# Optimization experiments

Measured on AMD Instinct MI355X. Metric: run time of the kernel, lower is better.

Reference implementation:

```python
import jax, jax.numpy as jnp
import numpy as np

K = 3
K2 = K * K


def conv2d(x, w, b, stride=1, pad=0):
    y = jax.lax.conv_general_dilated(
        x, w, (stride, stride), [(pad, pad), (pad, pad)],
        dimension_numbers=('NCHW', 'OIHW', 'NCHW'))
    return y + b[None, :, None, None]


def bilinear_gather(x, ys, xs):
    # x: [B,C,H,W]; ys,xs: [B,K2,H,W] float coords; zero outside bounds (torchvision deform_conv2d semantics)
    B, C, H, W = x.shape
    y0 = jnp.floor(ys)
    x0 = jnp.floor(xs)
    fy = (ys - y0)[:, None]  # [B,1,K2,H,W]
    fx = (xs - x0)[:, None]
    xf = x.reshape(B, C, H * W)

    def gather(yc, xc):
        valid = (yc >= 0) & (yc <= H - 1) & (xc >= 0) & (xc <= W - 1)
        yi = jnp.clip(yc, 0, H - 1).astype(jnp.int32)
        xi = jnp.clip(xc, 0, W - 1).astype(jnp.int32)
        idx = (yi * W + xi).reshape(B, 1, -1)
        g = jnp.take_along_axis(xf, idx, axis=2).reshape(B, C, K2, H, W)
        return g * valid[:, None].astype(x.dtype)

    g00 = gather(y0, x0)
    g01 = gather(y0, x0 + 1)
    g10 = gather(y0 + 1, x0)
    g11 = gather(y0 + 1, x0 + 1)
    return (g00 * (1 - fy) * (1 - fx) + g01 * (1 - fy) * fx
            + g10 * fy * (1 - fx) + g11 * fy * fx)


def deform_conv(x, w_off, b_off, w, b):
    # DCNv1: offsets predicted by a regular 3x3 conv, then 3x3 conv over bilinearly sampled taps
    B, C, H, W = x.shape
    pad = 1
    off = conv2d(x, w_off, b_off, pad=pad).reshape(B, K2, 2, H, W)  # (dy,dx) per tap
    ky, kx = jnp.meshgrid(jnp.arange(K), jnp.arange(K), indexing='ij')
    base_y = jnp.arange(H)[None, None, :, None] + (ky.reshape(K2) - pad)[None, :, None, None]
    base_x = jnp.arange(W)[None, None, None, :] + (kx.reshape(K2) - pad)[None, :, None, None]
    ys = base_y + off[:, :, 0]
    xs = base_x + off[:, :, 1]
    samples = bilinear_gather(x, ys, xs)  # [B,C,K2,H,W]
    out = jnp.einsum('bckhw,ock->bohw', samples, w.reshape(w.shape[0], C, K2))
    return out + b[None, :, None, None]


def band_high_mask(h, w):
    y, x = jnp.meshgrid(jnp.arange(h), jnp.arange(w), indexing='ij')
    d = jnp.sqrt(((y - h // 2) ** 2 + (x - w // 2) ** 2).astype(jnp.float32))
    return (d > h // 16).astype(jnp.float32)


def reference(x, w1, b1, ws, bs, wb, bb, woff, boff, wreg, breg, w2, b2):
    B, Cin, Hx, Wx = x.shape
    c0 = conv2d(x, w1, b1)                                  # 1x1 reduce
    c1 = conv2d(c0, ws, bs, stride=2, pad=0)                # 3x3 s2 p0 -> 111x111
    c1 = jax.lax.reduce_window(c1, -jnp.inf, jax.lax.max,
                               (1, 1, 7, 7), (1, 1, 3, 3), 'VALID')  # -> 35x35
    f = jnp.fft.fftshift(jnp.fft.fft2(c1, axes=(-2, -1)), axes=(-2, -1))
    mag = jnp.abs(f)
    phase = jnp.angle(f)
    h, w = mag.shape[-2], mag.shape[-1]
    hb = mag * band_high_mask(h, w)
    for l in range(3):  # fixed structural loop over the 3 DCN+ReLU blocks
        hb = jax.nn.relu(deform_conv(hb, woff[l], boff[l], wreg[l], breg[l]))
    rec = jax.lax.complex(hb * jnp.cos(phase), hb * jnp.sin(phase))
    rec = jnp.real(jnp.fft.ifft2(jnp.fft.ifftshift(rec, axes=(-2, -1)), axes=(-2, -1)))
    up = jax.image.resize(rec, (B, rec.shape[1], Hx, Wx), method='bilinear')  # align_corners=False
    c2 = jax.nn.sigmoid(conv2d(conv2d(c0, wb, bb) + up, w2, b2))
    return x * c2


def setup_inputs():
    key = jax.random.key(0)
    ks = jax.random.split(key, 8)
    B, Cin, H, W = 4, 256, 224, 224
    Cr = Cin // 8
    f32 = jnp.float32
    x = jax.random.normal(ks[0], (B, Cin, H, W), f32)
    w1 = jax.random.normal(ks[1], (Cr, Cin, 1, 1), f32) * 0.05
    b1 = jnp.zeros((Cr,), f32)
    ws = jax.random.normal(ks[2], (Cr, Cr, 3, 3), f32) * 0.05
    bs = jnp.zeros((Cr,), f32)
    wb = jax.random.normal(ks[3], (Cr, Cr, 1, 1), f32) * 0.05
    bb = jnp.zeros((Cr,), f32)
    woff = jax.random.normal(ks[4], (3, 2 * K2, Cr, 3, 3), f32) * 0.002  # small -> moderate offsets
    boff = jnp.zeros((3, 2 * K2), f32)
    wreg = jax.random.normal(ks[5], (3, Cr, Cr, 3, 3), f32) * 0.05
    breg = jnp.zeros((3, Cr), f32)
    w2 = jax.random.normal(ks[6], (Cin, Cr, 1, 1), f32) * 0.05
    b2 = jnp.zeros((Cin,), f32)
    return dict(x=x, w1=w1, b1=b1, ws=ws, bs=bs, wb=wb, bb=bb,
                woff=woff, boff=boff, wreg=wreg, breg=breg, w2=w2, b2=b2)
```

## Files before the change

### kernel.cpp

```cpp
#include <hip/hip_runtime.h>
#include <math.h>

#define PI_F 3.14159265358979323846f

#define BATCH 4
#define CIN 256
#define CR 32
#define H0 224
#define HW0 (224*224)
#define H1 111
#define HW1 (111*111)
#define HS 35
#define HWS (35*35)

typedef short bf16x8 __attribute__((ext_vector_type(8)));
typedef float f32x4 __attribute__((ext_vector_type(4)));
typedef unsigned int u32x4 __attribute__((ext_vector_type(4)));

__device__ inline unsigned pack2bf(float a, float b) {
  unsigned ua = __builtin_bit_cast(unsigned, a);
  unsigned ub = __builtin_bit_cast(unsigned, b);
  return ((ua + 0x8000u) >> 16) | (((ub + 0x8000u) & 0xFFFF0000u) | (((ub + 0x8000u) >> 16) << 16));
}

__device__ inline unsigned pack2(float a, float b) {
  unsigned ua = __builtin_bit_cast(unsigned, a);
  unsigned ub = __builtin_bit_cast(unsigned, b);
  return ((ua + 0x8000u) >> 16) | (((ub + 0x8000u) >> 16) << 16);
}

__device__ inline bf16x8 pack8(const float f[8]) {
  u32x4 u;
  u[0] = pack2(f[0], f[1]);
  u[1] = pack2(f[2], f[3]);
  u[2] = pack2(f[4], f[5]);
  u[3] = pack2(f[6], f[7]);
  return __builtin_bit_cast(bf16x8, u);
}

__global__ __launch_bounds__(256) void k_conv1x1(
    const float* __restrict__ x, const float* __restrict__ w1,
    const float* __restrict__ b1, float* __restrict__ c0) {
  int tid = threadIdx.x, lane = tid & 63, wid = tid >> 6;
  int l15 = lane & 15, lg = lane >> 4;
  int pxg = blockIdx.x * 256 + wid * 64;
  int b = pxg / HW0, p0 = pxg % HW0;
  bf16x8 A[2][8];
#pragma unroll
  for (int ct = 0; ct < 2; ++ct)
#pragma unroll
    for (int ks = 0; ks < 8; ++ks) {
      const float* wr = w1 + (ct * 16 + l15) * CIN + ks * 32 + lg * 8;
      float f[8];
      float4 a0 = *reinterpret_cast<const float4*>(wr);
      float4 a1 = *reinterpret_cast<const float4*>(wr + 4);
      f[0]=a0.x; f[1]=a0.y; f[2]=a0.z; f[3]=a0.w;
      f[4]=a1.x; f[5]=a1.y; f[6]=a1.z; f[7]=a1.w;
      A[ct][ks] = pack8(f);
    }
  f32x4 acc[2][4];
#pragma unroll
  for (int ct = 0; ct < 2; ++ct)
#pragma unroll
    for (int pt = 0; pt < 4; ++pt)
#pragma unroll
      for (int r = 0; r < 4; ++r) acc[ct][pt][r] = 0.f;
  const float* xb = x + (size_t)b * CIN * HW0 + p0 + l15;
  for (int ks = 0; ks < 8; ++ks) {
    bf16x8 Bf[4];
#pragma unroll
    for (int pt = 0; pt < 4; ++pt) {
      const float* xp = xb + (size_t)(ks * 32 + lg * 8) * HW0 + pt * 16;
      float f[8];
#pragma unroll
      for (int j = 0; j < 8; ++j) f[j] = xp[(size_t)j * HW0];
      Bf[pt] = pack8(f);
    }
#pragma unroll
    for (int ct = 0; ct < 2; ++ct)
#pragma unroll
      for (int pt = 0; pt < 4; ++pt)
        acc[ct][pt] = __builtin_amdgcn_mfma_f32_16x16x32_bf16(
            A[ct][ks], Bf[pt], acc[ct][pt], 0, 0, 0);
  }
#pragma unroll
  for (int ct = 0; ct < 2; ++ct) {
    float bias[4];
#pragma unroll
    for (int r = 0; r < 4; ++r) bias[r] = b1[ct * 16 + lg * 4 + r];
    float* ob = c0 + ((size_t)b * CR + ct * 16 + lg * 4) * HW0 + p0 + l15;
#pragma unroll
    for (int pt = 0; pt < 4; ++pt)
#pragma unroll
      for (int r = 0; r < 4; ++r)
        ob[(size_t)r * HW0 + pt * 16] = acc[ct][pt][r] + bias[r];
  }
}

#define PPR 56
#define PAIRS_B (H1 * PPR)
#define PAIRS_T (BATCH * PAIRS_B)
#define C3_THREADS (PAIRS_T * 4)
__global__ __launch_bounds__(256) void k_conv3x3s2(
    const float* __restrict__ c0, const float* __restrict__ wsw,
    const float* __restrict__ bs, float* __restrict__ c1) {
  __shared__ float wl[288 * 32];
  int tid = threadIdx.x;
  for (int i = tid; i < 9216; i += 256) {
    int o = i & 31, r = i >> 5;
    wl[i] = wsw[o * 288 + r];
  }
  __syncthreads();
  int T = blockIdx.x * 256 + tid;
  if (T >= C3_THREADS) return;
  int og = T / PAIRS_T;
  int pair = T % PAIRS_T;
  int b = pair / PAIRS_B;
  int pr = pair % PAIRS_B;
  int y = pr / PPR, xp = pr % PPR;
  bool tail = (xp == PPR - 1);
  const float* ibase = c0 + (size_t)b * CR * HW0 + (2 * y) * H0 + 4 * xp;
  float acc0[8], acc1[8];
#pragma unroll
  for (int j = 0; j < 8; ++j) { acc0[j] = 0.f; acc1[j] = 0.f; }
  for (int ci = 0; ci < CR; ++ci) {
    float p[3][5];
#pragma unroll
    for (int ky = 0; ky < 3; ++ky) {
      const float* rp = ibase + (size_t)ci * HW0 + ky * H0;
      float4 v = *reinterpret_cast<const float4*>(rp);
      p[ky][0] = v.x; p[ky][1] = v.y; p[ky][2] = v.z; p[ky][3] = v.w;
      p[ky][4] = tail ? 0.f : rp[4];
    }
    const float* wbase = &wl[ci * 9 * 32 + og * 8];
#pragma unroll
    for (int k = 0; k < 9; ++k) {
      int ky = k / 3, kx = k % 3;
      float4 wa = *reinterpret_cast<const float4*>(wbase + k * 32);
      float4 wc = *reinterpret_cast<const float4*>(wbase + k * 32 + 4);
      float wv[8] = {wa.x, wa.y, wa.z, wa.w, wc.x, wc.y, wc.z, wc.w};
      float pa = p[ky][kx], pb = p[ky][kx + 2];
#pragma unroll
      for (int j = 0; j < 8; ++j) {
        acc0[j] = fmaf(pa, wv[j], acc0[j]);
        acc1[j] = fmaf(pb, wv[j], acc1[j]);
      }
    }
  }
  float* ob = c1 + (size_t)b * CR * HW1 + y * H1 + 2 * xp;
  int o0 = og * 8;
#pragma unroll
  for (int j = 0; j < 8; ++j) {
    float bias = bs[o0 + j];
    ob[(size_t)(o0 + j) * HW1] = acc0[j] + bias;
    if (!tail) ob[(size_t)(o0 + j) * HW1 + 1] = acc1[j] + bias;
  }
}

__global__ __launch_bounds__(256) void k_maxpool(
    const float* __restrict__ c1, float* __restrict__ pool) {
  int idx = blockIdx.x * 256 + threadIdx.x;
  if (idx >= BATCH * CR * HWS) return;
  int ch = idx / HWS, r = idx % HWS;
  int y = r / HS, x = r % HS;
  const float* ip = c1 + (size_t)ch * HW1 + (3 * y) * H1 + 3 * x;
  float m = -INFINITY;
#pragma unroll
  for (int ky = 0; ky < 7; ++ky)
#pragma unroll
    for (int kx = 0; kx < 7; ++kx)
      m = fmaxf(m, ip[ky * H1 + kx]);
  pool[idx] = m;
}

__global__ __launch_bounds__(256) void k_fft(
    const float* __restrict__ pool, float* __restrict__ hb,
    float* __restrict__ cph, float* __restrict__ sph) {
  __shared__ float p[HWS];
  __shared__ float Tr[HWS], Ti[HWS];
  __shared__ float twc[HS], tws[HS];
  int img = blockIdx.x;
  const float* ip = pool + (size_t)img * HWS;
  for (int i = threadIdx.x; i < HWS; i += 256) p[i] = ip[i];
  if (threadIdx.x < HS) {
    float ang = -2.f * PI_F * (float)threadIdx.x / (float)HS;
    twc[threadIdx.x] = cosf(ang);
    tws[threadIdx.x] = sinf(ang);
  }
  __syncthreads();
  for (int i = threadIdx.x; i < HWS; i += 256) {
    int u = i / HS, xx = i % HS;
    float sr = 0.f, si = 0.f;
    int t = 0;
    for (int y = 0; y < HS; ++y) {
      float v = p[y * HS + xx];
      sr = fmaf(v, twc[t], sr);
      si = fmaf(v, tws[t], si);
      t += u; if (t >= HS) t -= HS;
    }
    Tr[i] = sr; Ti[i] = si;
  }
  __syncthreads();
  float* hp = hb + (size_t)img * HWS;
  float* cp = cph + (size_t)img * HWS;
  float* sp = sph + (size_t)img * HWS;
  for (int i = threadIdx.x; i < HWS; i += 256) {
    int oy = i / HS, ox = i % HS;
    int u = oy + 18; if (u >= HS) u -= HS;
    int v = ox + 18; if (v >= HS) v -= HS;
    float fr = 0.f, fi = 0.f;
    int t = 0;
    for (int xx = 0; xx < HS; ++xx) {
      float tr = Tr[u * HS + xx], ti = Ti[u * HS + xx];
      float c = twc[t], s = tws[t];
      fr += tr * c - ti * s;
      fi += tr * s + ti * c;
      t += v; if (t >= HS) t -= HS;
    }
    float mag = sqrtf(fr * fr + fi * fi);
    float ic = 1.f, is = 0.f;
    if (mag > 0.f) { ic = fr / mag; is = fi / mag; }
    int dy = oy - 17, dx = ox - 17;
    float m = (dy * dy + dx * dx > 4) ? 1.f : 0.f;
    hp[i] = mag * m;
    cp[i] = ic; sp[i] = is;
  }
}

__global__ __launch_bounds__(256) void k_dcn(
    const float* __restrict__ hin, float* __restrict__ hout,
    const float* __restrict__ woff, const float* __restrict__ boff,
    const float* __restrict__ wreg, const float* __restrict__ breg) {
  __shared__ float wo[18 * CR * 9];
  __shared__ float wr[CR * CR * 9];
  __shared__ float bo[18], br[CR];
  for (int i = threadIdx.x; i < 18 * CR * 9; i += 256) wo[i] = woff[i];
  for (int i = threadIdx.x; i < CR * CR * 9; i += 256) wr[i] = wreg[i];
  if (threadIdx.x < 18) bo[threadIdx.x] = boff[threadIdx.x];
  if (threadIdx.x < CR) br[threadIdx.x] = breg[threadIdx.x];
  __syncthreads();
  int pg = threadIdx.x >> 5;
  int sub = threadIdx.x & 31;
  int pid = blockIdx.x * 8 + pg;
  bool active = pid < BATCH * HWS;
  int b = pid / HWS, r = pid % HWS;
  int y = r / HS, x = r % HS;
  const float* ib = hin + (size_t)b * CR * HWS;
  float off[18];
#pragma unroll
  for (int j = 0; j < 18; ++j) off[j] = 0.f;
  if (active) {
    const float* ip = ib + (size_t)sub * HWS;
#pragma unroll
    for (int ky = 0; ky < 3; ++ky) {
      int yy = y + ky - 1;
      if (yy < 0 || yy > HS - 1) continue;
#pragma unroll
      for (int kx = 0; kx < 3; ++kx) {
        int xx = x + kx - 1;
        if (xx < 0 || xx > HS - 1) continue;
        float v = ip[yy * HS + xx];
#pragma unroll
        for (int j = 0; j < 18; ++j)
          off[j] = fmaf(v, wo[(j * CR + sub) * 9 + ky * 3 + kx], off[j]);
      }
    }
  }
#pragma unroll
  for (int d = 1; d < 32; d <<= 1)
#pragma unroll
    for (int j = 0; j < 18; ++j)
      off[j] += __shfl_xor(off[j], d);
#pragma unroll
  for (int j = 0; j < 18; ++j) off[j] += bo[j];
  float acc[CR];
#pragma unroll
  for (int o = 0; o < CR; ++o) acc[o] = 0.f;
  if (active) {
    const float* ip = ib + (size_t)sub * HWS;
#pragma unroll
    for (int k = 0; k < 9; ++k) {
      int ky = k / 3, kx = k % 3;
      float ysf = (float)(y + ky - 1) + off[2 * k];
      float xsf = (float)(x + kx - 1) + off[2 * k + 1];
      float y0 = floorf(ysf), x0 = floorf(xsf);
      float fy = ysf - y0, fx = xsf - x0;
      float y1 = y0 + 1.f, x1 = x0 + 1.f;
      bool vy0 = (y0 >= 0.f) && (y0 <= 34.f);
      bool vy1 = (y1 >= 0.f) && (y1 <= 34.f);
      bool vx0 = (x0 >= 0.f) && (x0 <= 34.f);
      bool vx1 = (x1 >= 0.f) && (x1 <= 34.f);
      int iy0 = (int)fminf(fmaxf(y0, 0.f), 34.f);
      int iy1 = (int)fminf(fmaxf(y1, 0.f), 34.f);
      int ix0 = (int)fminf(fmaxf(x0, 0.f), 34.f);
      int ix1 = (int)fminf(fmaxf(x1, 0.f), 34.f);
      float w00 = (vy0 && vx0) ? (1.f - fy) * (1.f - fx) : 0.f;
      float w01 = (vy0 && vx1) ? (1.f - fy) * fx : 0.f;
      float w10 = (vy1 && vx0) ? fy * (1.f - fx) : 0.f;
      float w11 = (vy1 && vx1) ? fy * fx : 0.f;
      float s = w00 * ip[iy0 * HS + ix0] + w01 * ip[iy0 * HS + ix1]
              + w10 * ip[iy1 * HS + ix0] + w11 * ip[iy1 * HS + ix1];
#pragma unroll
      for (int o = 0; o < CR; ++o)
        acc[o] = fmaf(s, wr[(o * CR + sub) * 9 + k], acc[o]);
    }
  }
#pragma unroll
  for (int d = 1; d < 32; d <<= 1)
#pragma unroll
    for (int o = 0; o < CR; ++o)
      acc[o] += __shfl_xor(acc[o], d);
  if (active) {
    float* ob = hout + (size_t)b * CR * HWS + r;
    float v = acc[sub] + br[sub];
    ob[(size_t)sub * HWS] = fmaxf(v, 0.f);
  }
}

__global__ __launch_bounds__(256) void k_ifft(
    const float* __restrict__ hb, const float* __restrict__ cph,
    const float* __restrict__ sph, float* __restrict__ rec) {
  __shared__ float Gr[HWS], Gi[HWS];
  __shared__ float Tr[HWS], Ti[HWS];
  __shared__ float twc[HS], tws[HS];
  int img = blockIdx.x;
  const float* hp = hb + (size_t)img * HWS;
  const float* cp = cph + (size_t)img * HWS;
  const float* sp = sph + (size_t)img * HWS;
  if (threadIdx.x < HS) {
    float ang = 2.f * PI_F * (float)threadIdx.x / (float)HS;
    twc[threadIdx.x] = cosf(ang);
    tws[threadIdx.x] = sinf(ang);
  }
  for (int i = threadIdx.x; i < HWS; i += 256) {
    int m = i / HS, n = i % HS;
    int sm = m + 17; if (sm >= HS) sm -= HS;
    int sn = n + 17; if (sn >= HS) sn -= HS;
    int si = sm * HS + sn;
    float h = hp[si];
    Gr[i] = h * cp[si];
    Gi[i] = h * sp[si];
  }
  __syncthreads();
  for (int i = threadIdx.x; i < HWS; i += 256) {
    int yy = i / HS, v = i % HS;
    float sr = 0.f, sii = 0.f;
    int t = 0;
    for (int u = 0; u < HS; ++u) {
      float gr = Gr[u * HS + v], gi = Gi[u * HS + v];
      float c = twc[t], s = tws[t];
      sr += gr * c - gi * s;
      sii += gr * s + gi * c;
      t += yy; if (t >= HS) t -= HS;
    }
    Tr[i] = sr; Ti[i] = sii;
  }
  __syncthreads();
  float* rp = rec + (size_t)img * HWS;
  const float inv = 1.f / (float)(HWS);
  for (int i = threadIdx.x; i < HWS; i += 256) {
    int yy = i / HS, xx = i % HS;
    float sr = 0.f;
    int t = 0;
    for (int v = 0; v < HS; ++v) {
      sr += Tr[yy * HS + v] * twc[t] - Ti[yy * HS + v] * tws[t];
      t += xx; if (t >= HS) t -= HS;
    }
    rp[i] = sr * inv;
  }
}

__global__ __launch_bounds__(256) void k_vmap(
    float* __restrict__ c0, const float* __restrict__ rec,
    const float* __restrict__ wb, const float* __restrict__ bb) {
  __shared__ float wblT[CR * CR];
  __shared__ float bbl[CR];
  int tid = threadIdx.x;
  for (int i = tid; i < CR * CR; i += 256) {
    int c = i / CR, cr = i % CR;
    wblT[i] = wb[cr * CR + c];
  }
  if (tid < CR) bbl[tid] = bb[tid];
  __syncthreads();
  int pix = blockIdx.x * 256 + tid;
  int b = pix / HW0, p = pix % HW0;
  int h = p / H0, wcol = p % H0;
  float* cb = c0 + (size_t)b * CR * HW0 + p;
  float cv[CR];
#pragma unroll
  for (int c = 0; c < CR; ++c) cv[c] = cb[(size_t)c * HW0];
  const float scale = (float)HS / (float)H0;
  float sy = ((float)h + 0.5f) * scale - 0.5f;
  float sx = ((float)wcol + 0.5f) * scale - 0.5f;
  float y0f = floorf(sy), x0f = floorf(sx);
  float fy = sy - y0f, fx = sx - x0f;
  int y0 = max(0, min(HS - 1, (int)y0f));
  int y1 = max(0, min(HS - 1, (int)y0f + 1));
  int x0 = max(0, min(HS - 1, (int)x0f));
  int x1 = max(0, min(HS - 1, (int)x0f + 1));
  float w00 = (1.f - fy) * (1.f - fx), w01 = (1.f - fy) * fx;
  float w10 = fy * (1.f - fx), w11 = fy * fx;
  const float* rb = rec + (size_t)b * CR * HWS;
  int i00 = y0 * HS + x0, i01 = y0 * HS + x1, i10 = y1 * HS + x0, i11 = y1 * HS + x1;
  float v[CR];
#pragma unroll
  for (int cr = 0; cr < CR; ++cr) {
    const float* rp = rb + (size_t)cr * HWS;
    v[cr] = bbl[cr] + w00 * rp[i00] + w01 * rp[i01] + w10 * rp[i10] + w11 * rp[i11];
  }
  for (int c = 0; c < CR; ++c) {
    float cvv = cv[c];
    const float4* wt = reinterpret_cast<const float4*>(&wblT[c * CR]);
#pragma unroll
    for (int q = 0; q < 8; ++q) {
      float4 wv = wt[q];
      v[q * 4 + 0] = fmaf(cvv, wv.x, v[q * 4 + 0]);
      v[q * 4 + 1] = fmaf(cvv, wv.y, v[q * 4 + 1]);
      v[q * 4 + 2] = fmaf(cvv, wv.z, v[q * 4 + 2]);
      v[q * 4 + 3] = fmaf(cvv, wv.w, v[q * 4 + 3]);
    }
  }
#pragma unroll
  for (int cr = 0; cr < CR; ++cr) cb[(size_t)cr * HW0] = v[cr];
}

__global__ __launch_bounds__(256) void k_final(
    const float* __restrict__ x, const float* __restrict__ vbuf,
    const float* __restrict__ w2, const float* __restrict__ b2,
    float* __restrict__ out) {
  int tid = threadIdx.x, lane = tid & 63, wid = tid >> 6;
  int l15 = lane & 15, lg = lane >> 4;
  int pxg = blockIdx.x * 256 + wid * 64;
  int b = pxg / HW0, p0 = pxg % HW0;
  int cb0 = blockIdx.y * 64;
  bf16x8 A[4];
#pragma unroll
  for (int ct = 0; ct < 4; ++ct) {
    const float* wr = w2 + (cb0 + ct * 16 + l15) * CR + lg * 8;
    float f[8];
    float4 a0 = *reinterpret_cast<const float4*>(wr);
    float4 a1 = *reinterpret_cast<const float4*>(wr + 4);
    f[0]=a0.x; f[1]=a0.y; f[2]=a0.z; f[3]=a0.w;
    f[4]=a1.x; f[5]=a1.y; f[6]=a1.z; f[7]=a1.w;
    A[ct] = pack8(f);
  }
  const float* vb = vbuf + (size_t)b * CR * HW0 + p0 + l15;
  bf16x8 Bf[4];
#pragma unroll
  for (int pt = 0; pt < 4; ++pt) {
    const float* vp = vb + (size_t)(lg * 8) * HW0 + pt * 16;
    float f[8];
#pragma unroll
    for (int j = 0; j < 8; ++j) f[j] = vp[(size_t)j * HW0];
    Bf[pt] = pack8(f);
  }
  f32x4 acc[4][4];
#pragma unroll
  for (int ct = 0; ct < 4; ++ct)
#pragma unroll
    for (int pt = 0; pt < 4; ++pt)
#pragma unroll
      for (int r = 0; r < 4; ++r) acc[ct][pt][r] = 0.f;
#pragma unroll
  for (int ct = 0; ct < 4; ++ct)
#pragma unroll
    for (int pt = 0; pt < 4; ++pt)
      acc[ct][pt] = __builtin_amdgcn_mfma_f32_16x16x32_bf16(
          A[ct], Bf[pt], acc[ct][pt], 0, 0, 0);
#pragma unroll
  for (int ct = 0; ct < 4; ++ct) {
    float bias[4];
#pragma unroll
    for (int r = 0; r < 4; ++r) bias[r] = b2[cb0 + ct * 16 + lg * 4 + r];
    const float* xb = x + ((size_t)b * CIN + cb0 + ct * 16 + lg * 4) * HW0 + p0 + l15;
    float* ob = out + ((size_t)b * CIN + cb0 + ct * 16 + lg * 4) * HW0 + p0 + l15;
#pragma unroll
    for (int pt = 0; pt < 4; ++pt)
#pragma unroll
      for (int r = 0; r < 4; ++r) {
        float s = acc[ct][pt][r] + bias[r];
        float g = __builtin_amdgcn_rcpf(1.f + __expf(-s));
        ob[(size_t)r * HW0 + pt * 16] = xb[(size_t)r * HW0 + pt * 16] * g;
      }
  }
}

extern "C" void kernel_launch(void* const* d_in, const int* in_sizes, int n_in,
                              void* d_out, int out_size, void* d_ws, size_t ws_size,
                              hipStream_t stream) {
  const float* x    = (const float*)d_in[0];
  const float* w1   = (const float*)d_in[1];
  const float* b1   = (const float*)d_in[2];
  const float* wsw  = (const float*)d_in[3];
  const float* bs   = (const float*)d_in[4];
  const float* wb   = (const float*)d_in[5];
  const float* bb   = (const float*)d_in[6];
  const float* woff = (const float*)d_in[7];
  const float* boff = (const float*)d_in[8];
  const float* wreg = (const float*)d_in[9];
  const float* breg = (const float*)d_in[10];
  const float* w2   = (const float*)d_in[11];
  const float* b2   = (const float*)d_in[12];
  float* out = (float*)d_out;

  float* ws_f = (float*)d_ws;
  float* c0   = ws_f;
  float* c1   = c0 + (size_t)BATCH * CR * HW0;
  float* pool = c1 + (size_t)BATCH * CR * HW1;
  float* hbA  = pool + (size_t)BATCH * CR * HWS;
  float* hbB  = hbA + (size_t)BATCH * CR * HWS;
  float* cph  = hbB + (size_t)BATCH * CR * HWS;
  float* sph  = cph + (size_t)BATCH * CR * HWS;
  float* rec  = sph + (size_t)BATCH * CR * HWS;

  k_conv1x1<<<BATCH * HW0 / 256, 256, 0, stream>>>(x, w1, b1, c0);
  k_conv3x3s2<<<(C3_THREADS + 255) / 256, 256, 0, stream>>>(c0, wsw, bs, c1);
  k_maxpool<<<(BATCH * CR * HWS + 255) / 256, 256, 0, stream>>>(c1, pool);
  k_fft<<<BATCH * CR, 256, 0, stream>>>(pool, hbA, cph, sph);
  k_dcn<<<(BATCH * HWS + 7) / 8, 256, 0, stream>>>(hbA, hbB, woff, boff, wreg, breg);
  k_dcn<<<(BATCH * HWS + 7) / 8, 256, 0, stream>>>(hbB, hbA, woff + 5184, boff + 18, wreg + 9216, breg + 32);
  k_dcn<<<(BATCH * HWS + 7) / 8, 256, 0, stream>>>(hbA, hbB, woff + 2 * 5184, boff + 36, wreg + 2 * 9216, breg + 64);
  k_ifft<<<BATCH * CR, 256, 0, stream>>>(hbB, cph, sph, rec);
  k_vmap<<<(BATCH * HW0) / 256, 256, 0, stream>>>(c0, rec, wb, bb);
  dim3 gf(BATCH * HW0 / 256, 4);
  k_final<<<gf, 256, 0, stream>>>(x, c0, w2, b2, out);
}
```

Baseline: 342.5 us.

## Fold wb 1x1 conv into conv1x1 weights, fuse vmap into final and maxpool into FFT

A new prep kernel precomputes wb·w1 and the combined bias, so conv1x1 produces both c0 and v0 = wb·c0+bb in one pass over x, using extra MFMA tiles. The separate vmap kernel is gone: k_final now adds the bilinear upsample of rec to v0 on the fly before its 1x1 MFMA, and covers 128 output channels per block, which halves the blockIdx.y dimension. Maxpool is computed inside the FFT kernel's load stage. These changes remove a full read and write of c0 and two kernel launches, at the cost of an extra 32-channel output buffer written by conv1x1 and more register pressure in conv1x1 and k_final.

```diff
diff --git a/kernel.cpp b/kernel.cpp
--- a/kernel.cpp
+++ b/kernel.cpp
@@ -17,12 +17,6 @@
 typedef float f32x4 __attribute__((ext_vector_type(4)));
 typedef unsigned int u32x4 __attribute__((ext_vector_type(4)));
 
-__device__ inline unsigned pack2bf(float a, float b) {
-  unsigned ua = __builtin_bit_cast(unsigned, a);
-  unsigned ub = __builtin_bit_cast(unsigned, b);
-  return ((ua + 0x8000u) >> 16) | (((ub + 0x8000u) & 0xFFFF0000u) | (((ub + 0x8000u) >> 16) << 16));
-}
-
 __device__ inline unsigned pack2(float a, float b) {
   unsigned ua = __builtin_bit_cast(unsigned, a);
   unsigned ub = __builtin_bit_cast(unsigned, b);
@@ -38,57 +32,89 @@
   return __builtin_bit_cast(bf16x8, u);
 }
 
+__global__ __launch_bounds__(256) void k_prep(
+    const float* __restrict__ w1, const float* __restrict__ b1,
+    const float* __restrict__ wb, const float* __restrict__ bb,
+    float* __restrict__ Wcat, float* __restrict__ bias_v) {
+  __shared__ float wbl[32 * 32];
+  int t = threadIdx.x;
+  for (int i = t; i < 1024; i += 256) wbl[i] = wb[i];
+  __syncthreads();
+  float col[32];
+#pragma unroll
+  for (int m = 0; m < 32; ++m) col[m] = w1[m * CIN + t];
+#pragma unroll
+  for (int o = 0; o < 32; ++o) {
+    float s = 0.f;
+#pragma unroll
+    for (int m = 0; m < 32; ++m) s = fmaf(wbl[o * 32 + m], col[m], s);
+    Wcat[o * CIN + t] = s;
+  }
+  if (t < 32) {
+    float s = bb[t];
+#pragma unroll
+    for (int m = 0; m < 32; ++m) s = fmaf(wbl[t * 32 + m], b1[m], s);
+    bias_v[t] = s;
+  }
+}
+
 __global__ __launch_bounds__(256) void k_conv1x1(
     const float* __restrict__ x, const float* __restrict__ w1,
-    const float* __restrict__ b1, float* __restrict__ c0) {
+    const float* __restrict__ b1, const float* __restrict__ Wcat,
+    const float* __restrict__ bias_v,
+    float* __restrict__ c0, float* __restrict__ v0) {
   int tid = threadIdx.x, lane = tid & 63, wid = tid >> 6;
   int l15 = lane & 15, lg = lane >> 4;
   int pxg = blockIdx.x * 256 + wid * 64;
   int b = pxg / HW0, p0 = pxg % HW0;
-  bf16x8 A[2][8];
-#pragma unroll
-  for (int ct = 0; ct < 2; ++ct)
-#pragma unroll
-    for (int ks = 0; ks < 8; ++ks) {
-      const float* wr = w1 + (ct * 16 + l15) * CIN + ks * 32 + lg * 8;
+  f32x4 acc[4][4];
+#pragma unroll
+  for (int ct = 0; ct < 4; ++ct)
+#pragma unroll
+    for (int pt = 0; pt < 4; ++pt)
+#pragma unroll
+      for (int r = 0; r < 4; ++r) acc[ct][pt][r] = 0.f;
+  const float* xb = x + (size_t)b * CIN * HW0 + p0 + l15;
+  for (int ks = 0; ks < 8; ++ks) {
+    bf16x8 Bf[4];
+#pragma unroll
+    for (int pt = 0; pt < 4; ++pt) {
+      const float* xp = xb + (size_t)(ks * 32 + lg * 8) * HW0 + pt * 16;
+      float f[8];
+#pragma unroll
+      for (int j = 0; j < 8; ++j) f[j] = xp[(size_t)j * HW0];
+      Bf[pt] = pack8(f);
+    }
+    bf16x8 A[4];
+#pragma unroll
+    for (int ct = 0; ct < 4; ++ct) {
+      const float* base = (ct < 2)
+          ? w1 + (ct * 16 + l15) * CIN
+          : Wcat + ((ct - 2) * 16 + l15) * CIN;
+      const float* wr = base + ks * 32 + lg * 8;
       float f[8];
       float4 a0 = *reinterpret_cast<const float4*>(wr);
       float4 a1 = *reinterpret_cast<const float4*>(wr + 4);
       f[0]=a0.x; f[1]=a0.y; f[2]=a0.z; f[3]=a0.w;
       f[4]=a1.x; f[5]=a1.y; f[6]=a1.z; f[7]=a1.w;
-      A[ct][ks] = pack8(f);
-    }
-  f32x4 acc[2][4];
-#pragma unroll
-  for (int ct = 0; ct < 2; ++ct)
-#pragma unroll
-    for (int pt = 0; pt < 4; ++pt)
-#pragma unroll
-      for (int r = 0; r < 4; ++r) acc[ct][pt][r] = 0.f;
-  const float* xb = x + (size_t)b * CIN * HW0 + p0 + l15;
-  for (int ks = 0; ks < 8; ++ks) {
-    bf16x8 Bf[4];
-#pragma unroll
-    for (int pt = 0; pt < 4; ++pt) {
-      const float* xp = xb + (size_t)(ks * 32 + lg * 8) * HW0 + pt * 16;
-      float f[8];
-#pragma unroll
-      for (int j = 0; j < 8; ++j) f[j] = xp[(size_t)j * HW0];
-      Bf[pt] = pack8(f);
-    }
-#pragma unroll
-    for (int ct = 0; ct < 2; ++ct)
+      A[ct] = pack8(f);
+    }
+#pragma unroll
+    for (int ct = 0; ct < 4; ++ct)
 #pragma unroll
       for (int pt = 0; pt < 4; ++pt)
         acc[ct][pt] = __builtin_amdgcn_mfma_f32_16x16x32_bf16(
-            A[ct][ks], Bf[pt], acc[ct][pt], 0, 0, 0);
-  }
-#pragma unroll
-  for (int ct = 0; ct < 2; ++ct) {
+            A[ct], Bf[pt], acc[ct][pt], 0, 0, 0);
+  }
+#pragma unroll
+  for (int ct = 0; ct < 4; ++ct) {
+    int co = (ct & 1) * 16 + lg * 4;
     float bias[4];
 #pragma unroll
-    for (int r = 0; r < 4; ++r) bias[r] = b1[ct * 16 + lg * 4 + r];
-    float* ob = c0 + ((size_t)b * CR + ct * 16 + lg * 4) * HW0 + p0 + l15;
+    for (int r = 0; r < 4; ++r)
+      bias[r] = (ct < 2) ? b1[co + r] : bias_v[co + r];
+    float* dst = (ct < 2) ? c0 : v0;
+    float* ob = dst + ((size_t)b * CR + co) * HW0 + p0 + l15;
 #pragma unroll
     for (int pt = 0; pt < 4; ++pt)
 #pragma unroll
@@ -157,31 +183,25 @@
   }
 }
 
-__global__ __launch_bounds__(256) void k_maxpool(
-    const float* __restrict__ c1, float* __restrict__ pool) {
-  int idx = blockIdx.x * 256 + threadIdx.x;
-  if (idx >= BATCH * CR * HWS) return;
-  int ch = idx / HWS, r = idx % HWS;
-  int y = r / HS, x = r % HS;
-  const float* ip = c1 + (size_t)ch * HW1 + (3 * y) * H1 + 3 * x;
-  float m = -INFINITY;
-#pragma unroll
-  for (int ky = 0; ky < 7; ++ky)
-#pragma unroll
-    for (int kx = 0; kx < 7; ++kx)
-      m = fmaxf(m, ip[ky * H1 + kx]);
-  pool[idx] = m;
-}
-
 __global__ __launch_bounds__(256) void k_fft(
-    const float* __restrict__ pool, float* __restrict__ hb,
+    const float* __restrict__ c1, float* __restrict__ hb,
     float* __restrict__ cph, float* __restrict__ sph) {
   __shared__ float p[HWS];
   __shared__ float Tr[HWS], Ti[HWS];
   __shared__ float twc[HS], tws[HS];
   int img = blockIdx.x;
-  const float* ip = pool + (size_t)img * HWS;
-  for (int i = threadIdx.x; i < HWS; i += 256) p[i] = ip[i];
+  const float* cb = c1 + (size_t)img * HW1;
+  for (int i = threadIdx.x; i < HWS; i += 256) {
+    int y = i / HS, x = i % HS;
+    const float* ip = cb + (3 * y) * H1 + 3 * x;
+    float m = -INFINITY;
+#pragma unroll
+    for (int ky = 0; ky < 7; ++ky)
+#pragma unroll
+      for (int kx = 0; kx < 7; ++kx)
+        m = fmaxf(m, ip[ky * H1 + kx]);
+    p[i] = m;
+  }
   if (threadIdx.x < HS) {
     float ang = -2.f * PI_F * (float)threadIdx.x / (float)HS;
     twc[threadIdx.x] = cosf(ang);
@@ -370,118 +390,89 @@
   }
 }
 
-__global__ __launch_bounds__(256) void k_vmap(
-    float* __restrict__ c0, const float* __restrict__ rec,
-    const float* __restrict__ wb, const float* __restrict__ bb) {
-  __shared__ float wblT[CR * CR];
-  __shared__ float bbl[CR];
-  int tid = threadIdx.x;
-  for (int i = tid; i < CR * CR; i += 256) {
-    int c = i / CR, cr = i % CR;
-    wblT[i] = wb[cr * CR + c];
-  }
-  if (tid < CR) bbl[tid] = bb[tid];
-  __syncthreads();
-  int pix = blockIdx.x * 256 + tid;
-  int b = pix / HW0, p = pix % HW0;
-  int h = p / H0, wcol = p % H0;
-  float* cb = c0 + (size_t)b * CR * HW0 + p;
-  float cv[CR];
-#pragma unroll
-  for (int c = 0; c < CR; ++c) cv[c] = cb[(size_t)c * HW0];
-  const float scale = (float)HS / (float)H0;
-  float sy = ((float)h + 0.5f) * scale - 0.5f;
-  float sx = ((float)wcol + 0.5f) * scale - 0.5f;
-  float y0f = floorf(sy), x0f = floorf(sx);
-  float fy = sy - y0f, fx = sx - x0f;
-  int y0 = max(0, min(HS - 1, (int)y0f));
-  int y1 = max(0, min(HS - 1, (int)y0f + 1));
-  int x0 = max(0, min(HS - 1, (int)x0f));
-  int x1 = max(0, min(HS - 1, (int)x0f + 1));
-  float w00 = (1.f - fy) * (1.f - fx), w01 = (1.f - fy) * fx;
-  float w10 = fy * (1.f - fx), w11 = fy * fx;
-  const float* rb = rec + (size_t)b * CR * HWS;
-  int i00 = y0 * HS + x0, i01 = y0 * HS + x1, i10 = y1 * HS + x0, i11 = y1 * HS + x1;
-  float v[CR];
-#pragma unroll
-  for (int cr = 0; cr < CR; ++cr) {
-    const float* rp = rb + (size_t)cr * HWS;
-    v[cr] = bbl[cr] + w00 * rp[i00] + w01 * rp[i01] + w10 * rp[i10] + w11 * rp[i11];
-  }
-  for (int c = 0; c < CR; ++c) {
-    float cvv = cv[c];
-    const float4* wt = reinterpret_cast<const float4*>(&wblT[c * CR]);
-#pragma unroll
-    for (int q = 0; q < 8; ++q) {
-      float4 wv = wt[q];
-      v[q * 4 + 0] = fmaf(cvv, wv.x, v[q * 4 + 0]);
-      v[q * 4 + 1] = fmaf(cvv, wv.y, v[q * 4 + 1]);
-      v[q * 4 + 2] = fmaf(cvv, wv.z, v[q * 4 + 2]);
-      v[q * 4 + 3] = fmaf(cvv, wv.w, v[q * 4 + 3]);
-    }
-  }
-#pragma unroll
-  for (int cr = 0; cr < CR; ++cr) cb[(size_t)cr * HW0] = v[cr];
-}
-
 __global__ __launch_bounds__(256) void k_final(
-    const float* __restrict__ x, const float* __restrict__ vbuf,
+    const float* __restrict__ x, const float* __restrict__ v0buf,
+    const float* __restrict__ rec,
     const float* __restrict__ w2, const float* __restrict__ b2,
     float* __restrict__ out) {
   int tid = threadIdx.x, lane = tid & 63, wid = tid >> 6;
   int l15 = lane & 15, lg = lane >> 4;
   int pxg = blockIdx.x * 256 + wid * 64;
   int b = pxg / HW0, p0 = pxg % HW0;
-  int cb0 = blockIdx.y * 64;
-  bf16x8 A[4];
-#pragma unroll
-  for (int ct = 0; ct < 4; ++ct) {
-    const float* wr = w2 + (cb0 + ct * 16 + l15) * CR + lg * 8;
+  int cb0 = blockIdx.y * 128;
+  const float* rb = rec + (size_t)b * CR * HWS;
+  const float* vb = v0buf + (size_t)b * CR * HW0 + p0 + l15;
+  const float scale = (float)HS / (float)H0;
+  bf16x8 Bf[4];
+#pragma unroll
+  for (int pt = 0; pt < 4; ++pt) {
+    int p = p0 + pt * 16 + l15;
+    int h = p / H0, wc = p % H0;
+    float sy = ((float)h + 0.5f) * scale - 0.5f;
+    float sx = ((float)wc + 0.5f) * scale - 0.5f;
+    float y0f = floorf(sy), x0f = floorf(sx);
+    float fy = sy - y0f, fx = sx - x0f;
+    int y0 = max(0, min(HS - 1, (int)y0f));
+    int y1 = max(0, min(HS - 1, (int)y0f + 1));
+    int x0 = max(0, min(HS - 1, (int)x0f));
+    int x1 = max(0, min(HS - 1, (int)x0f + 1));
+    float w00 = (1.f - fy) * (1.f - fx), w01 = (1.f - fy) * fx;
+    float w10 = fy * (1.f - fx), w11 = fy * fx;
+    int i00 = y0 * HS + x0, i01 = y0 * HS + x1;
+    int i10 = y1 * HS + x0, i11 = y1 * HS + x1;
     float f[8];
-    float4 a0 = *reinterpret_cast<const float4*>(wr);
-    float4 a1 = *reinterpret_cast<const float4*>(wr + 4);
-    f[0]=a0.x; f[1]=a0.y; f[2]=a0.z; f[3]=a0.w;
-    f[4]=a1.x; f[5]=a1.y; f[6]=a1.z; f[7]=a1.w;
-    A[ct] = pack8(f);
-  }
-  const float* vb = vbuf + (size_t)b * CR * HW0 + p0 + l15;
-  bf16x8 Bf[4];
-#pragma unroll
-  for (int pt = 0; pt < 4; ++pt) {
-    const float* vp = vb + (size_t)(lg * 8) * HW0 + pt * 16;
-    float f[8];
-#pragma unroll
-    for (int j = 0; j < 8; ++j) f[j] = vp[(size_t)j * HW0];
+#pragma unroll
+    for (int j = 0; j < 8; ++j) {
+      const float* rp = rb + (size_t)(lg * 8 + j) * HWS;
+      float u = w00 * rp[i00] + w01 * rp[i01] + w10 * rp[i10] + w11 * rp[i11];
+      f[j] = vb[(size_t)(lg * 8 + j) * HW0 + pt * 16] + u;
+    }
     Bf[pt] = pack8(f);
   }
-  f32x4 acc[4][4];
-#pragma unroll
-  for (int ct = 0; ct < 4; ++ct)
-#pragma unroll
-    for (int pt = 0; pt < 4; ++pt)
-#pragma unroll
-      for (int r = 0; r < 4; ++r) acc[ct][pt][r] = 0.f;
-#pragma unroll
-  for (int ct = 0; ct < 4; ++ct)
-#pragma unroll
-    for (int pt = 0; pt < 4; ++pt)
-      acc[ct][pt] = __builtin_amdgcn_mfma_f32_16x16x32_bf16(
-          A[ct], Bf[pt], acc[ct][pt], 0, 0, 0);
-#pragma unroll
-  for (int ct = 0; ct < 4; ++ct) {
-    float bias[4];
-#pragma unroll
-    for (int r = 0; r < 4; ++r) bias[r] = b2[cb0 + ct * 16 + lg * 4 + r];
-    const float* xb = x + ((size_t)b * CIN + cb0 + ct * 16 + lg * 4) * HW0 + p0 + l15;
-    float* ob = out + ((size_t)b * CIN + cb0 + ct * 16 + lg * 4) * HW0 + p0 + l15;
-#pragma unroll
-    for (int pt = 0; pt < 4; ++pt)
-#pragma unroll
-      for (int r = 0; r < 4; ++r) {
-        float s = acc[ct][pt][r] + bias[r];
-        float g = __builtin_amdgcn_rcpf(1.f + __expf(-s));
-        ob[(size_t)r * HW0 + pt * 16] = xb[(size_t)r * HW0 + pt * 16] * g;
-      }
+#pragma unroll
+  for (int chunk = 0; chunk < 2; ++chunk) {
+    int ctb = cb0 + chunk * 64;
+    bf16x8 A[4];
+#pragma unroll
+    for (int ct = 0; ct < 4; ++ct) {
+      const float* wr = w2 + (ctb + ct * 16 + l15) * CR + lg * 8;
+      float f[8];
+      float4 a0 = *reinterpret_cast<const float4*>(wr);
+      float4 a1 = *reinterpret_cast<const float4*>(wr + 4);
+      f[0]=a0.x; f[1]=a0.y; f[2]=a0.z; f[3]=a0.w;
+      f[4]=a1.x; f[5]=a1.y; f[6]=a1.z; f[7]=a1.w;
+      A[ct] = pack8(f);
+    }
+    f32x4 acc[4][4];
+#pragma unroll
+    for (int ct = 0; ct < 4; ++ct)
+#pragma unroll
+      for (int pt = 0; pt < 4; ++pt)
+#pragma unroll
+        for (int r = 0; r < 4; ++r) acc[ct][pt][r] = 0.f;
+#pragma unroll
+    for (int ct = 0; ct < 4; ++ct)
+#pragma unroll
+      for (int pt = 0; pt < 4; ++pt)
+        acc[ct][pt] = __builtin_amdgcn_mfma_f32_16x16x32_bf16(
+            A[ct], Bf[pt], acc[ct][pt], 0, 0, 0);
+#pragma unroll
+    for (int ct = 0; ct < 4; ++ct) {
+      int co = ctb + ct * 16 + lg * 4;
+      float bias[4];
+#pragma unroll
+      for (int r = 0; r < 4; ++r) bias[r] = b2[co + r];
+      const float* xb = x + ((size_t)b * CIN + co) * HW0 + p0 + l15;
+      float* ob = out + ((size_t)b * CIN + co) * HW0 + p0 + l15;
+#pragma unroll
+      for (int pt = 0; pt < 4; ++pt)
+#pragma unroll
+        for (int r = 0; r < 4; ++r) {
+          float s = acc[ct][pt][r] + bias[r];
+          float g = __builtin_amdgcn_rcpf(1.f + __expf(-s));
+          ob[(size_t)r * HW0 + pt * 16] = xb[(size_t)r * HW0 + pt * 16] * g;
+        }
+    }
   }
 }
 
@@ -505,23 +496,24 @@
 
   float* ws_f = (float*)d_ws;
   float* c0   = ws_f;
-  float* c1   = c0 + (size_t)BATCH * CR * HW0;
-  float* pool = c1 + (size_t)BATCH * CR * HW1;
-  float* hbA  = pool + (size_t)BATCH * CR * HWS;
+  float* v0   = c0 + (size_t)BATCH * CR * HW0;
+  float* c1   = v0 + (size_t)BATCH * CR * HW0;
+  float* hbA  = c1 + (size_t)BATCH * CR * HW1;
   float* hbB  = hbA + (size_t)BATCH * CR * HWS;
   float* cph  = hbB + (size_t)BATCH * CR * HWS;
   float* sph  = cph + (size_t)BATCH * CR * HWS;
   float* rec  = sph + (size_t)BATCH * CR * HWS;
-
-  k_conv1x1<<<BATCH * HW0 / 256, 256, 0, stream>>>(x, w1, b1, c0);
+  float* Wcat = rec + (size_t)BATCH * CR * HWS;
+  float* bias_v = Wcat + 32 * CIN;
+
+  k_prep<<<1, 256, 0, stream>>>(w1, b1, wb, bb, Wcat, bias_v);
+  k_conv1x1<<<BATCH * HW0 / 256, 256, 0, stream>>>(x, w1, b1, Wcat, bias_v, c0, v0);
   k_conv3x3s2<<<(C3_THREADS + 255) / 256, 256, 0, stream>>>(c0, wsw, bs, c1);
-  k_maxpool<<<(BATCH * CR * HWS + 255) / 256, 256, 0, stream>>>(c1, pool);
-  k_fft<<<BATCH * CR, 256, 0, stream>>>(pool, hbA, cph, sph);
+  k_fft<<<BATCH * CR, 256, 0, stream>>>(c1, hbA, cph, sph);
   k_dcn<<<(BATCH * HWS + 7) / 8, 256, 0, stream>>>(hbA, hbB, woff, boff, wreg, breg);
   k_dcn<<<(BATCH * HWS + 7) / 8, 256, 0, stream>>>(hbB, hbA, woff + 5184, boff + 18, wreg + 9216, breg + 32);
   k_dcn<<<(BATCH * HWS + 7) / 8, 256, 0, stream>>>(hbA, hbB, woff + 2 * 5184, boff + 36, wreg + 2 * 9216, breg + 64);
   k_ifft<<<BATCH * CR, 256, 0, stream>>>(hbB, cph, sph, rec);
-  k_vmap<<<(BATCH * HW0) / 256, 256, 0, stream>>>(c0, rec, wb, bb);
-  dim3 gf(BATCH * HW0 / 256, 4);
-  k_final<<<gf, 256, 0, stream>>>(x, c0, w2, b2, out);
-}
+  dim3 gf(BATCH * HW0 / 256, 2);
+  k_final<<<gf, 256, 0, stream>>>(x, v0, rec, w2, b2, out);
+}
```

Result: no change. 349.2 us (+2.0%).
